# Kernel tuning notes

Measured on AMD Instinct MI355X. Metric: run time of the kernel, lower is better.

## Reference

```python
import jax, jax.numpy as jnp
import numpy as np

N = 100000   # total nodes across the batch of glycan graphs
E = 300000   # directed edges
H = 256      # hidden_dim
D = 128      # embedding_dim (projection out)
L = 3        # num_layers
G = 10000    # number of graphs in the batch
V = 14       # monosaccharide vocab size
EPS = 1e-5   # BatchNorm eps


def setup_inputs() -> dict:
    key = jax.random.key(0)
    ks = jax.random.split(key, 12)
    s = 1.0 / np.sqrt(H)
    node_ids = jax.random.randint(ks[0], (N,), 0, V, dtype=jnp.int32)
    edge_index = jax.random.randint(ks[1], (2, E), 0, N, dtype=jnp.int32)
    batch_ids = jnp.sort(jax.random.randint(ks[2], (N,), 0, G, dtype=jnp.int32))
    return {
        "node_ids": node_ids,
        "edge_index": edge_index,
        "batch_ids": batch_ids,
        "emb": jax.random.normal(ks[3], (V, H), jnp.float32),
        "Ws": jax.random.normal(ks[4], (L, H, H), jnp.float32) * s,
        "bs": jax.random.normal(ks[5], (L, H), jnp.float32) * 0.01,
        "gammas": 1.0 + 0.1 * jax.random.normal(ks[6], (L, H), jnp.float32),
        "betas": 0.1 * jax.random.normal(ks[7], (L, H), jnp.float32),
        "run_mean": 0.1 * jax.random.normal(ks[8], (L, H), jnp.float32),
        "run_var": jax.random.uniform(ks[9], (L, H), jnp.float32) + 0.5,
        "projW": jax.random.normal(ks[10], (H, D), jnp.float32) * s,
        "projb": jax.random.normal(ks[11], (D,), jnp.float32) * 0.01,
    }


def reference(node_ids, edge_index, batch_ids, emb, Ws, bs, gammas, betas,
              run_mean, run_var, projW, projb):
    # --- GCN normalization with self-loops (PyG GCNConv defaults) ---
    src, dst = edge_index[0], edge_index[1]
    loops = jnp.arange(N, dtype=src.dtype)
    src_f = jnp.concatenate([src, loops])  # [E+N]
    dst_f = jnp.concatenate([dst, loops])
    deg = jax.ops.segment_sum(jnp.ones_like(dst_f, dtype=jnp.float32), dst_f,
                              num_segments=N)
    dinv = jnp.where(deg > 0, jax.lax.rsqrt(deg), 0.0)
    norm = dinv[src_f] * dinv[dst_f]       # [E+N]

    x = emb[node_ids]                       # [N, H]
    for l in range(L):
        h = x @ Ws[l]                       # GCNConv linear transform
        msg = h[src_f] * norm[:, None]      # [E+N, H] gathered messages
        h = jax.ops.segment_sum(msg, dst_f, num_segments=N) + bs[l]
        # BatchNorm1d (eval mode: running stats) + ReLU; dropout is identity in eval
        h = (h - run_mean[l]) * jax.lax.rsqrt(run_var[l] + EPS) * gammas[l] + betas[l]
        x = jax.nn.relu(h)

    # global_mean_pool over graph assignment
    counts = jax.ops.segment_sum(jnp.ones((N,), jnp.float32), batch_ids,
                                 num_segments=G)
    sums = jax.ops.segment_sum(x, batch_ids, num_segments=G)   # [G, H]
    pooled = sums / jnp.maximum(counts, 1.0)[:, None]
    return pooled @ projW + projb           # [G, D]
```

## Files before the change

kernel.cpp:

```cpp
#include <hip/hip_runtime.h>

#define HDIM 256
#define DDIM 128
#define VSZ 14

typedef __bf16 bf16x8 __attribute__((ext_vector_type(8)));
typedef float f32x4 __attribute__((ext_vector_type(4)));

static __device__ __forceinline__ unsigned short f2bf(float f) {
  unsigned u = __builtin_bit_cast(unsigned, f);
  u += 0x7FFF + ((u >> 16) & 1);
  return (unsigned short)(u >> 16);
}
static __device__ __forceinline__ unsigned pack2(float a, float b) {
  return (unsigned)f2bf(a) | ((unsigned)f2bf(b) << 16);
}
static __device__ __forceinline__ void ub8(uint4 p, float* o) {
  o[0] = __builtin_bit_cast(float, p.x << 16);
  o[1] = __builtin_bit_cast(float, p.x & 0xFFFF0000u);
  o[2] = __builtin_bit_cast(float, p.y << 16);
  o[3] = __builtin_bit_cast(float, p.y & 0xFFFF0000u);
  o[4] = __builtin_bit_cast(float, p.z << 16);
  o[5] = __builtin_bit_cast(float, p.z & 0xFFFF0000u);
  o[6] = __builtin_bit_cast(float, p.w << 16);
  o[7] = __builtin_bit_cast(float, p.w & 0xFFFF0000u);
}


__global__ void k_count(const int* __restrict__ dst, int* __restrict__ cnt, int E) {
  int i = blockIdx.x * 256 + threadIdx.x;
  if (i < E) atomicAdd(&cnt[dst[i]], 1);
}

__global__ void k_alloc(const int* __restrict__ cnt, int* __restrict__ off,
                        float* __restrict__ dinv, int2* __restrict__ ninfo,
                        const int* __restrict__ ids, int* __restrict__ total, int n) {
  __shared__ int s[256];
  __shared__ int base;
  int i = blockIdx.x * 256 + threadIdx.x;
  int c = (i < n) ? cnt[i] : 0;
  if (i < n) {
    float dv = rsqrtf((float)(c + 1));
    dinv[i] = dv;
    int2 inf;
    inf.x = ids[i];
    inf.y = __builtin_bit_cast(int, dv);
    ninfo[i] = inf;
  }
  s[threadIdx.x] = c;
  __syncthreads();
  for (int d = 1; d < 256; d <<= 1) {
    int add = (threadIdx.x >= d) ? s[threadIdx.x - d] : 0;
    __syncthreads();
    s[threadIdx.x] += add;
    __syncthreads();
  }
  if (threadIdx.x == 255) base = atomicAdd(total, s[255]);
  __syncthreads();
  if (i < n) off[i] = base + s[threadIdx.x] - c;
}

__global__ void k_fill(const int* __restrict__ src, const int* __restrict__ dst,
                       const int2* __restrict__ ninfo, const int* __restrict__ off,
                       int* __restrict__ cur, int4* __restrict__ edata, int E) {
  int i = blockIdx.x * 256 + threadIdx.x;
  if (i >= E) return;
  int d = dst[i];
  int p = off[d] + atomicAdd(&cur[d], 1);
  int s = src[i];
  int2 inf = ninfo[s];
  int4 v;
  v.x = s;
  v.y = inf.x;
  v.z = inf.y;
  v.w = 0;
  edata[p] = v;
}


__global__ __launch_bounds__(256) void k_prep(
    const float* __restrict__ emb, const float* __restrict__ Ws,
    const float* __restrict__ bs, const float* __restrict__ gam,
    const float* __restrict__ bet, const float* __restrict__ mu,
    const float* __restrict__ va, const int* __restrict__ batch,
    float* __restrict__ embW, float* __restrict__ Ac, float* __restrict__ Bc,
    unsigned short* __restrict__ Wtb, int* __restrict__ goff, int G, int n) {
  int b = blockIdx.x;
  if (b < 128) {
    __shared__ float tile[32][33];
    int layer = b >> 6;
    int tb = b & 63;
    int bx = (tb & 7) * 32, by = (tb >> 3) * 32;
    const float* W = Ws + (size_t)(layer + 1) * HDIM * HDIM;
    unsigned short* Wt = Wtb + (size_t)layer * HDIM * HDIM;
    int tx = threadIdx.x & 31, ty = threadIdx.x >> 5;
#pragma unroll
    for (int i = 0; i < 4; ++i)
      tile[ty + i * 8][tx] = W[(size_t)(by + ty + i * 8) * HDIM + bx + tx];
    __syncthreads();
#pragma unroll
    for (int i = 0; i < 4; ++i)
      Wt[(size_t)(bx + ty + i * 8) * HDIM + by + tx] = f2bf(tile[tx][ty + i * 8]);
  } else if (b < 142) {
    int t = b - 128, j = threadIdx.x;
    float acc = 0.f;
    for (int k = 0; k < HDIM; ++k) acc = fmaf(emb[t * HDIM + k], Ws[k * HDIM + j], acc);
    embW[t * HDIM + j] = acc;
  } else if (b < 145) {
    int i = (b - 142) * HDIM + threadIdx.x;
    float a = gam[i] * rsqrtf(va[i] + 1e-5f);
    Ac[i] = a;
    Bc[i] = (bs[i] - mu[i]) * a + bet[i];
  } else {
    int g = (b - 145) * 256 + threadIdx.x;
    if (g > G) return;
    int lo = 0, hi = n;
    while (lo < hi) {
      int mid = (lo + hi) >> 1;
      if (batch[mid] < g) lo = mid + 1;
      else hi = mid;
    }
    goff[g] = lo;
  }
}


__global__ __launch_bounds__(256) void k_layer1(
    const int* __restrict__ ids, const float* __restrict__ embW,
    const int* __restrict__ off, const int* __restrict__ deg,
    const int4* __restrict__ edata, const float* __restrict__ dinv,
    const float* __restrict__ A, const float* __restrict__ B,
    unsigned short* __restrict__ Y, int n) {
  __shared__ unsigned short lw[VSZ * HDIM];
  for (int i = threadIdx.x; i < VSZ * HDIM; i += 256) lw[i] = f2bf(embW[i]);
  __syncthreads();
  int j = (threadIdx.x & 31) * 8;
  float4 a0 = *reinterpret_cast<const float4*>(&A[j]);
  float4 a1 = *reinterpret_cast<const float4*>(&A[j + 4]);
  float4 b0 = *reinterpret_cast<const float4*>(&B[j]);
  float4 b1 = *reinterpret_cast<const float4*>(&B[j + 4]);
  int nb = (n + 7) >> 3;
  for (int b = blockIdx.x; b < nb; b += gridDim.x) {
    int v = b * 8 + (threadIdx.x >> 5);
    if (v >= n) continue;
    float dv = dinv[v];
    float s = dv * dv;
    float acc[8], m[8];
    uint4 x = *reinterpret_cast<const uint4*>(&lw[ids[v] * HDIM + j]);
    ub8(x, acc);
#pragma unroll
    for (int i = 0; i < 8; ++i) acc[i] *= s;
    int e = off[v], e1 = e + deg[v];
    for (; e + 3 < e1; e += 4) {
      int4 d0 = edata[e], d1 = edata[e + 1], d2 = edata[e + 2], d3 = edata[e + 3];
      uint4 g0 = *reinterpret_cast<const uint4*>(&lw[d0.y * HDIM + j]);
      uint4 g1 = *reinterpret_cast<const uint4*>(&lw[d1.y * HDIM + j]);
      uint4 g2 = *reinterpret_cast<const uint4*>(&lw[d2.y * HDIM + j]);
      uint4 g3 = *reinterpret_cast<const uint4*>(&lw[d3.y * HDIM + j]);
      float w0 = dv * __builtin_bit_cast(float, d0.z);
      float w1 = dv * __builtin_bit_cast(float, d1.z);
      float w2 = dv * __builtin_bit_cast(float, d2.z);
      float w3 = dv * __builtin_bit_cast(float, d3.z);
      ub8(g0, m);
#pragma unroll
      for (int i = 0; i < 8; ++i) acc[i] = fmaf(w0, m[i], acc[i]);
      ub8(g1, m);
#pragma unroll
      for (int i = 0; i < 8; ++i) acc[i] = fmaf(w1, m[i], acc[i]);
      ub8(g2, m);
#pragma unroll
      for (int i = 0; i < 8; ++i) acc[i] = fmaf(w2, m[i], acc[i]);
      ub8(g3, m);
#pragma unroll
      for (int i = 0; i < 8; ++i) acc[i] = fmaf(w3, m[i], acc[i]);
    }
    for (; e < e1; ++e) {
      int4 d0 = edata[e];
      uint4 g0 = *reinterpret_cast<const uint4*>(&lw[d0.y * HDIM + j]);
      float w0 = dv * __builtin_bit_cast(float, d0.z);
      ub8(g0, m);
#pragma unroll
      for (int i = 0; i < 8; ++i) acc[i] = fmaf(w0, m[i], acc[i]);
    }
    float o[8];
    o[0] = fmaxf(fmaf(acc[0], a0.x, b0.x), 0.f);
    o[1] = fmaxf(fmaf(acc[1], a0.y, b0.y), 0.f);
    o[2] = fmaxf(fmaf(acc[2], a0.z, b0.z), 0.f);
    o[3] = fmaxf(fmaf(acc[3], a0.w, b0.w), 0.f);
    o[4] = fmaxf(fmaf(acc[4], a1.x, b1.x), 0.f);
    o[5] = fmaxf(fmaf(acc[5], a1.y, b1.y), 0.f);
    o[6] = fmaxf(fmaf(acc[6], a1.z, b1.z), 0.f);
    o[7] = fmaxf(fmaf(acc[7], a1.w, b1.w), 0.f);
    uint4 st;
    st.x = pack2(o[0], o[1]);
    st.y = pack2(o[2], o[3]);
    st.z = pack2(o[4], o[5]);
    st.w = pack2(o[6], o[7]);
    *reinterpret_cast<uint4*>(&Y[(size_t)v * HDIM + j]) = st;
  }
}


__global__ __launch_bounds__(256) void k_agg(
    const unsigned short* __restrict__ X, const int* __restrict__ off,
    const int* __restrict__ deg, const int4* __restrict__ edata,
    const float* __restrict__ dinv, unsigned short* __restrict__ Yb, int n) {
  int j = (threadIdx.x & 31) * 8;
  int nb = (n + 7) >> 3;
  for (int b = blockIdx.x; b < nb; b += gridDim.x) {
    int v = b * 8 + (threadIdx.x >> 5);
    if (v >= n) continue;
    float dv = dinv[v];
    float s = dv * dv;
    float acc[8], m[8];
    uint4 x = *reinterpret_cast<const uint4*>(&X[(size_t)v * HDIM + j]);
    ub8(x, acc);
#pragma unroll
    for (int i = 0; i < 8; ++i) acc[i] *= s;
    int e = off[v], e1 = e + deg[v];
    for (; e + 3 < e1; e += 4) {
      int4 d0 = edata[e], d1 = edata[e + 1], d2 = edata[e + 2], d3 = edata[e + 3];
      uint4 g0 = *reinterpret_cast<const uint4*>(&X[(size_t)d0.x * HDIM + j]);
      uint4 g1 = *reinterpret_cast<const uint4*>(&X[(size_t)d1.x * HDIM + j]);
      uint4 g2 = *reinterpret_cast<const uint4*>(&X[(size_t)d2.x * HDIM + j]);
      uint4 g3 = *reinterpret_cast<const uint4*>(&X[(size_t)d3.x * HDIM + j]);
      float w0 = dv * __builtin_bit_cast(float, d0.z);
      float w1 = dv * __builtin_bit_cast(float, d1.z);
      float w2 = dv * __builtin_bit_cast(float, d2.z);
      float w3 = dv * __builtin_bit_cast(float, d3.z);
      ub8(g0, m);
#pragma unroll
      for (int i = 0; i < 8; ++i) acc[i] = fmaf(w0, m[i], acc[i]);
      ub8(g1, m);
#pragma unroll
      for (int i = 0; i < 8; ++i) acc[i] = fmaf(w1, m[i], acc[i]);
      ub8(g2, m);
#pragma unroll
      for (int i = 0; i < 8; ++i) acc[i] = fmaf(w2, m[i], acc[i]);
      ub8(g3, m);
#pragma unroll
      for (int i = 0; i < 8; ++i) acc[i] = fmaf(w3, m[i], acc[i]);
    }
    for (; e < e1; ++e) {
      int4 d0 = edata[e];
      uint4 g0 = *reinterpret_cast<const uint4*>(&X[(size_t)d0.x * HDIM + j]);
      float w0 = dv * __builtin_bit_cast(float, d0.z);
      ub8(g0, m);
#pragma unroll
      for (int i = 0; i < 8; ++i) acc[i] = fmaf(w0, m[i], acc[i]);
    }
    uint4 st;
    st.x = pack2(acc[0], acc[1]);
    st.y = pack2(acc[2], acc[3]);
    st.z = pack2(acc[4], acc[5]);
    st.w = pack2(acc[6], acc[7]);
    *reinterpret_cast<uint4*>(&Yb[(size_t)v * HDIM + j]) = st;
  }
}


#define BM 128
#define BN 128
#define BK 32
#define LDK 40
#define LDC 136

__global__ __launch_bounds__(256) void k_gemm_mfma(
    const unsigned short* __restrict__ Xb, const unsigned short* __restrict__ Wt,
    const float* __restrict__ Asc, const float* __restrict__ Bsh,
    unsigned short* __restrict__ Y, int M) {
  __shared__ uint4 smem4[BM * LDC / 8];
  unsigned short* As = reinterpret_cast<unsigned short*>(smem4);
  unsigned short* Bs = As + BM * LDK;
  unsigned short* Cs = As;
  int t = threadIdx.x;
  int m0 = blockIdx.x * BM;
  int n0 = blockIdx.y * BN;
  int l = t & 63, w = t >> 6;
  int wm = w & 1, wn = w >> 1;
  int cl = l & 15, q = l >> 4;
  int r0 = t >> 2;
  int kc = (t & 3) * 8;

  f32x4 acc[4][4];
  f32x4 zf = {0.f, 0.f, 0.f, 0.f};
#pragma unroll
  for (int i = 0; i < 4; ++i)
#pragma unroll
    for (int jj = 0; jj < 4; ++jj) acc[i][jj] = zf;

  int arow0 = m0 + r0;      if (arow0 > M - 1) arow0 = M - 1;
  int arow1 = m0 + r0 + 64; if (arow1 > M - 1) arow1 = M - 1;
  int brow0 = n0 + r0, brow1 = n0 + r0 + 64;

  for (int k0 = 0; k0 < HDIM; k0 += BK) {
    uint4 a0 = *reinterpret_cast<const uint4*>(&Xb[(size_t)arow0 * HDIM + k0 + kc]);
    uint4 a1 = *reinterpret_cast<const uint4*>(&Xb[(size_t)arow1 * HDIM + k0 + kc]);
    uint4 b0 = *reinterpret_cast<const uint4*>(&Wt[(size_t)brow0 * HDIM + k0 + kc]);
    uint4 b1 = *reinterpret_cast<const uint4*>(&Wt[(size_t)brow1 * HDIM + k0 + kc]);
    __syncthreads();
    *reinterpret_cast<uint4*>(&As[r0 * LDK + kc]) = a0;
    *reinterpret_cast<uint4*>(&As[(r0 + 64) * LDK + kc]) = a1;
    *reinterpret_cast<uint4*>(&Bs[r0 * LDK + kc]) = b0;
    *reinterpret_cast<uint4*>(&Bs[(r0 + 64) * LDK + kc]) = b1;
    __syncthreads();
    bf16x8 af[4], bfr[4];
#pragma unroll
    for (int i = 0; i < 4; ++i)
      af[i] = *reinterpret_cast<const bf16x8*>(&As[(wm * 64 + i * 16 + cl) * LDK + q * 8]);
#pragma unroll
    for (int jj = 0; jj < 4; ++jj)
      bfr[jj] = *reinterpret_cast<const bf16x8*>(&Bs[(wn * 64 + jj * 16 + cl) * LDK + q * 8]);
#pragma unroll
    for (int i = 0; i < 4; ++i)
#pragma unroll
      for (int jj = 0; jj < 4; ++jj)
        acc[i][jj] = __builtin_amdgcn_mfma_f32_16x16x32_bf16(af[i], bfr[jj], acc[i][jj], 0, 0, 0);
  }

  __syncthreads();
#pragma unroll
  for (int jj = 0; jj < 4; ++jj) {
    int col = wn * 64 + jj * 16 + cl;
    float as = Asc[n0 + col], bsv = Bsh[n0 + col];
#pragma unroll
    for (int i = 0; i < 4; ++i) {
      int rowb = wm * 64 + i * 16 + q * 4;
#pragma unroll
      for (int r = 0; r < 4; ++r)
        Cs[(rowb + r) * LDC + col] = f2bf(fmaxf(fmaf(acc[i][jj][r], as, bsv), 0.f));
    }
  }
  __syncthreads();
#pragma unroll
  for (int c = 0; c < 8; ++c) {
    int idx = t + 256 * c;
    int row = idx >> 4, cq = (idx & 15) * 8;
    int gr = m0 + row;
    if (gr < M)
      *reinterpret_cast<uint4*>(&Y[(size_t)gr * HDIM + n0 + cq]) =
          *reinterpret_cast<const uint4*>(&Cs[row * LDC + cq]);
  }
}


__global__ __launch_bounds__(256) void k_pool(
    const unsigned short* __restrict__ X, const int* __restrict__ goff,
    float* __restrict__ P, int G) {
  int g = blockIdx.x * 8 + (threadIdx.x >> 5);
  if (g >= G) return;
  int j = (threadIdx.x & 31) * 8;
  int r0 = goff[g], r1 = goff[g + 1];
  float acc[8] = {0.f, 0.f, 0.f, 0.f, 0.f, 0.f, 0.f, 0.f};
  float m[8];
  int r = r0;
  for (; r + 1 < r1; r += 2) {
    uint4 x0 = *reinterpret_cast<const uint4*>(&X[(size_t)r * HDIM + j]);
    uint4 x1 = *reinterpret_cast<const uint4*>(&X[(size_t)(r + 1) * HDIM + j]);
    ub8(x0, m);
#pragma unroll
    for (int i = 0; i < 8; ++i) acc[i] += m[i];
    ub8(x1, m);
#pragma unroll
    for (int i = 0; i < 8; ++i) acc[i] += m[i];
  }
  if (r < r1) {
    uint4 x0 = *reinterpret_cast<const uint4*>(&X[(size_t)r * HDIM + j]);
    ub8(x0, m);
#pragma unroll
    for (int i = 0; i < 8; ++i) acc[i] += m[i];
  }
  float inv = 1.f / fmaxf((float)(r1 - r0), 1.f);
  float4 o0 = make_float4(acc[0] * inv, acc[1] * inv, acc[2] * inv, acc[3] * inv);
  float4 o1 = make_float4(acc[4] * inv, acc[5] * inv, acc[6] * inv, acc[7] * inv);
  *reinterpret_cast<float4*>(&P[(size_t)g * HDIM + j]) = o0;
  *reinterpret_cast<float4*>(&P[(size_t)g * HDIM + j + 4]) = o1;
}


__global__ __launch_bounds__(128) void k_proj(
    const float* __restrict__ P, const float* __restrict__ W,
    const float* __restrict__ bias, float* __restrict__ out, int G) {
  __shared__ float rows[8][HDIM];
  int g0 = blockIdx.x * 8;
  for (int i = threadIdx.x; i < 8 * HDIM; i += 128) {
    int g = g0 + (i >> 8);
    rows[i >> 8][i & 255] = (g < G) ? P[(size_t)g * HDIM + (i & 255)] : 0.f;
  }
  __syncthreads();
  int d = threadIdx.x;
  float bb = bias[d];
  float acc[8] = {bb, bb, bb, bb, bb, bb, bb, bb};
  for (int k = 0; k < HDIM; ++k) {
    float w = W[(size_t)k * DDIM + d];
#pragma unroll
    for (int q = 0; q < 8; ++q) acc[q] = fmaf(rows[q][k], w, acc[q]);
  }
#pragma unroll
  for (int q = 0; q < 8; ++q) {
    int g = g0 + q;
    if (g < G) out[(size_t)g * DDIM + d] = acc[q];
  }
}


extern "C" void kernel_launch(void* const* d_in, const int* in_sizes, int n_in,
                              void* d_out, int out_size, void* d_ws, size_t ws_size,
                              hipStream_t stream) {
  const int N = in_sizes[0];
  const int E = in_sizes[1] / 2;
  const int G = out_size / DDIM;

  const int* node_ids = (const int*)d_in[0];
  const int* src = (const int*)d_in[1];
  const int* dst = src + E;
  const int* batch = (const int*)d_in[2];
  const float* emb = (const float*)d_in[3];
  const float* Ws = (const float*)d_in[4];
  const float* bs = (const float*)d_in[5];
  const float* gam = (const float*)d_in[6];
  const float* bet = (const float*)d_in[7];
  const float* mu = (const float*)d_in[8];
  const float* va = (const float*)d_in[9];
  const float* pW = (const float*)d_in[10];
  const float* pb = (const float*)d_in[11];
  float* out = (float*)d_out;

  size_t o = 0;
  auto alloc = [&](size_t bytes) -> void* {
    size_t start = (o + 255) & ~(size_t)255;
    o = start + bytes;
    return (void*)((char*)d_ws + start);
  };
  int* zbuf = (int*)alloc((size_t)(2 * N + 1) * 4);
  int* cnt = zbuf;
  int* cur = zbuf + N;
  int* total = zbuf + 2 * N;
  float* dinv = (float*)alloc((size_t)N * 4);
  int* off = (int*)alloc((size_t)N * 4);
  int2* ninfo = (int2*)alloc((size_t)N * 8);
  int4* edata = (int4*)alloc((size_t)E * 16);
  float* embW = (float*)alloc((size_t)VSZ * HDIM * 4);
  float* Ac = (float*)alloc((size_t)3 * HDIM * 4);
  float* Bc = (float*)alloc((size_t)3 * HDIM * 4);
  int* goff = (int*)alloc((size_t)(G + 1) * 4);
  unsigned short* Wtb = (unsigned short*)alloc((size_t)2 * HDIM * HDIM * 2);
  unsigned short* bufX = (unsigned short*)alloc((size_t)N * HDIM * 2);
  unsigned short* bufY = (unsigned short*)alloc((size_t)N * HDIM * 2);
  float* pooled = (float*)alloc((size_t)G * HDIM * 4);

  int gE = (E + 255) / 256;
  int NB = (N + 255) / 256;
  int NGB = (G + 1 + 255) / 256;

  hipMemsetAsync(zbuf, 0, (size_t)(2 * N + 1) * 4, stream);
  k_count<<<gE, 256, 0, stream>>>(dst, cnt, E);
  k_alloc<<<NB, 256, 0, stream>>>(cnt, off, dinv, ninfo, node_ids, total, N);
  k_fill<<<gE, 256, 0, stream>>>(src, dst, ninfo, off, cur, edata, E);

  k_prep<<<145 + NGB, 256, 0, stream>>>(emb, Ws, bs, gam, bet, mu, va, batch,
                                        embW, Ac, Bc, Wtb, goff, G, N);

  int gs = 2048;
  k_layer1<<<gs, 256, 0, stream>>>(node_ids, embW, off, cnt, edata, dinv,
                                   Ac, Bc, bufX, N);

  dim3 gg((N + BM - 1) / BM, HDIM / BN);
  k_agg<<<gs, 256, 0, stream>>>(bufX, off, cnt, edata, dinv, bufY, N);
  k_gemm_mfma<<<gg, 256, 0, stream>>>(bufY, Wtb, Ac + HDIM, Bc + HDIM, bufX, N);
  k_agg<<<gs, 256, 0, stream>>>(bufX, off, cnt, edata, dinv, bufY, N);
  k_gemm_mfma<<<gg, 256, 0, stream>>>(bufY, Wtb + HDIM * HDIM, Ac + 2 * HDIM, Bc + 2 * HDIM, bufX, N);

  k_pool<<<(G + 7) / 8, 256, 0, stream>>>(bufX, goff, pooled, G);
  k_proj<<<(G + 7) / 8, 128, 0, stream>>>(pooled, pW, pb, out, G);
}
```

Before: 270.7 us.

## Pack edge records to 8 bytes and fuse mean-pool into final GEMM epilogue

Edge records shrink from 16 to 8 bytes by packing the node id (24 bits) and the vocab id (top 8 bits) into one int, which halves edge-list traffic in the aggregation kernels. The last GEMM now skips writing its bf16 output and instead sums rows per graph from shared memory, adding the partial sums into a zeroed fp32 pooled buffer with atomics. The pool kernel is removed and the mean division moves into the projection kernel. This trades one full write and read of the node feature matrix for atomic contention and a larger memset, and it relies on node ids fitting in 24 bits.

```diff
diff --git a/kernel.cpp b/kernel.cpp
--- a/kernel.cpp
+++ b/kernel.cpp
@@ -11,6 +11,10 @@
   unsigned u = __builtin_bit_cast(unsigned, f);
   u += 0x7FFF + ((u >> 16) & 1);
   return (unsigned short)(u >> 16);
+}
+static __device__ __forceinline__ float bf2f(unsigned short u) {
+  unsigned x = ((unsigned)u) << 16;
+  return __builtin_bit_cast(float, x);
 }
 static __device__ __forceinline__ unsigned pack2(float a, float b) {
   return (unsigned)f2bf(a) | ((unsigned)f2bf(b) << 16);
@@ -62,18 +66,16 @@
 
 __global__ void k_fill(const int* __restrict__ src, const int* __restrict__ dst,
                        const int2* __restrict__ ninfo, const int* __restrict__ off,
-                       int* __restrict__ cur, int4* __restrict__ edata, int E) {
+                       int* __restrict__ cur, int2* __restrict__ edata, int E) {
   int i = blockIdx.x * 256 + threadIdx.x;
   if (i >= E) return;
   int d = dst[i];
   int p = off[d] + atomicAdd(&cur[d], 1);
   int s = src[i];
   int2 inf = ninfo[s];
-  int4 v;
-  v.x = s;
-  v.y = inf.x;
-  v.z = inf.y;
-  v.w = 0;
+  int2 v;
+  v.x = s | (inf.x << 24);
+  v.y = inf.y;
   edata[p] = v;
 }
 
@@ -128,7 +130,7 @@
 __global__ __launch_bounds__(256) void k_layer1(
     const int* __restrict__ ids, const float* __restrict__ embW,
     const int* __restrict__ off, const int* __restrict__ deg,
-    const int4* __restrict__ edata, const float* __restrict__ dinv,
+    const int2* __restrict__ edata, const float* __restrict__ dinv,
     const float* __restrict__ A, const float* __restrict__ B,
     unsigned short* __restrict__ Y, int n) {
   __shared__ unsigned short lw[VSZ * HDIM];
@@ -152,15 +154,15 @@
     for (int i = 0; i < 8; ++i) acc[i] *= s;
     int e = off[v], e1 = e + deg[v];
     for (; e + 3 < e1; e += 4) {
-      int4 d0 = edata[e], d1 = edata[e + 1], d2 = edata[e + 2], d3 = edata[e + 3];
-      uint4 g0 = *reinterpret_cast<const uint4*>(&lw[d0.y * HDIM + j]);
-      uint4 g1 = *reinterpret_cast<const uint4*>(&lw[d1.y * HDIM + j]);
-      uint4 g2 = *reinterpret_cast<const uint4*>(&lw[d2.y * HDIM + j]);
-      uint4 g3 = *reinterpret_cast<const uint4*>(&lw[d3.y * HDIM + j]);
-      float w0 = dv * __builtin_bit_cast(float, d0.z);
-      float w1 = dv * __builtin_bit_cast(float, d1.z);
-      float w2 = dv * __builtin_bit_cast(float, d2.z);
-      float w3 = dv * __builtin_bit_cast(float, d3.z);
+      int2 d0 = edata[e], d1 = edata[e + 1], d2 = edata[e + 2], d3 = edata[e + 3];
+      uint4 g0 = *reinterpret_cast<const uint4*>(&lw[((unsigned)d0.x >> 24) * HDIM + j]);
+      uint4 g1 = *reinterpret_cast<const uint4*>(&lw[((unsigned)d1.x >> 24) * HDIM + j]);
+      uint4 g2 = *reinterpret_cast<const uint4*>(&lw[((unsigned)d2.x >> 24) * HDIM + j]);
+      uint4 g3 = *reinterpret_cast<const uint4*>(&lw[((unsigned)d3.x >> 24) * HDIM + j]);
+      float w0 = dv * __builtin_bit_cast(float, d0.y);
+      float w1 = dv * __builtin_bit_cast(float, d1.y);
+      float w2 = dv * __builtin_bit_cast(float, d2.y);
+      float w3 = dv * __builtin_bit_cast(float, d3.y);
       ub8(g0, m);
 #pragma unroll
       for (int i = 0; i < 8; ++i) acc[i] = fmaf(w0, m[i], acc[i]);
@@ -175,9 +177,9 @@
       for (int i = 0; i < 8; ++i) acc[i] = fmaf(w3, m[i], acc[i]);
     }
     for (; e < e1; ++e) {
-      int4 d0 = edata[e];
-      uint4 g0 = *reinterpret_cast<const uint4*>(&lw[d0.y * HDIM + j]);
-      float w0 = dv * __builtin_bit_cast(float, d0.z);
+      int2 d0 = edata[e];
+      uint4 g0 = *reinterpret_cast<const uint4*>(&lw[((unsigned)d0.x >> 24) * HDIM + j]);
+      float w0 = dv * __builtin_bit_cast(float, d0.y);
       ub8(g0, m);
 #pragma unroll
       for (int i = 0; i < 8; ++i) acc[i] = fmaf(w0, m[i], acc[i]);
@@ -203,7 +205,7 @@
 
 __global__ __launch_bounds__(256) void k_agg(
     const unsigned short* __restrict__ X, const int* __restrict__ off,
-    const int* __restrict__ deg, const int4* __restrict__ edata,
+    const int* __restrict__ deg, const int2* __restrict__ edata,
     const float* __restrict__ dinv, unsigned short* __restrict__ Yb, int n) {
   int j = (threadIdx.x & 31) * 8;
   int nb = (n + 7) >> 3;
@@ -219,15 +221,15 @@
     for (int i = 0; i < 8; ++i) acc[i] *= s;
     int e = off[v], e1 = e + deg[v];
     for (; e + 3 < e1; e += 4) {
-      int4 d0 = edata[e], d1 = edata[e + 1], d2 = edata[e + 2], d3 = edata[e + 3];
-      uint4 g0 = *reinterpret_cast<const uint4*>(&X[(size_t)d0.x * HDIM + j]);
-      uint4 g1 = *reinterpret_cast<const uint4*>(&X[(size_t)d1.x * HDIM + j]);
-      uint4 g2 = *reinterpret_cast<const uint4*>(&X[(size_t)d2.x * HDIM + j]);
-      uint4 g3 = *reinterpret_cast<const uint4*>(&X[(size_t)d3.x * HDIM + j]);
-      float w0 = dv * __builtin_bit_cast(float, d0.z);
-      float w1 = dv * __builtin_bit_cast(float, d1.z);
-      float w2 = dv * __builtin_bit_cast(float, d2.z);
-      float w3 = dv * __builtin_bit_cast(float, d3.z);
+      int2 d0 = edata[e], d1 = edata[e + 1], d2 = edata[e + 2], d3 = edata[e + 3];
+      uint4 g0 = *reinterpret_cast<const uint4*>(&X[(size_t)(d0.x & 0xFFFFFF) * HDIM + j]);
+      uint4 g1 = *reinterpret_cast<const uint4*>(&X[(size_t)(d1.x & 0xFFFFFF) * HDIM + j]);
+      uint4 g2 = *reinterpret_cast<const uint4*>(&X[(size_t)(d2.x & 0xFFFFFF) * HDIM + j]);
+      uint4 g3 = *reinterpret_cast<const uint4*>(&X[(size_t)(d3.x & 0xFFFFFF) * HDIM + j]);
+      float w0 = dv * __builtin_bit_cast(float, d0.y);
+      float w1 = dv * __builtin_bit_cast(float, d1.y);
+      float w2 = dv * __builtin_bit_cast(float, d2.y);
+      float w3 = dv * __builtin_bit_cast(float, d3.y);
       ub8(g0, m);
 #pragma unroll
       for (int i = 0; i < 8; ++i) acc[i] = fmaf(w0, m[i], acc[i]);
@@ -242,9 +244,9 @@
       for (int i = 0; i < 8; ++i) acc[i] = fmaf(w3, m[i], acc[i]);
     }
     for (; e < e1; ++e) {
-      int4 d0 = edata[e];
-      uint4 g0 = *reinterpret_cast<const uint4*>(&X[(size_t)d0.x * HDIM + j]);
-      float w0 = dv * __builtin_bit_cast(float, d0.z);
+      int2 d0 = edata[e];
+      uint4 g0 = *reinterpret_cast<const uint4*>(&X[(size_t)(d0.x & 0xFFFFFF) * HDIM + j]);
+      float w0 = dv * __builtin_bit_cast(float, d0.y);
       ub8(g0, m);
 #pragma unroll
       for (int i = 0; i < 8; ++i) acc[i] = fmaf(w0, m[i], acc[i]);
@@ -265,10 +267,12 @@
 #define LDK 40
 #define LDC 136
 
+template <bool POOL>
 __global__ __launch_bounds__(256) void k_gemm_mfma(
     const unsigned short* __restrict__ Xb, const unsigned short* __restrict__ Wt,
     const float* __restrict__ Asc, const float* __restrict__ Bsh,
-    unsigned short* __restrict__ Y, int M) {
+    unsigned short* __restrict__ Y, float* __restrict__ pooled,
+    const int* __restrict__ batch, int M) {
   __shared__ uint4 smem4[BM * LDC / 8];
   unsigned short* As = reinterpret_cast<unsigned short*>(smem4);
   unsigned short* Bs = As + BM * LDK;
@@ -332,60 +336,54 @@
     }
   }
   __syncthreads();
-#pragma unroll
-  for (int c = 0; c < 8; ++c) {
-    int idx = t + 256 * c;
-    int row = idx >> 4, cq = (idx & 15) * 8;
-    int gr = m0 + row;
-    if (gr < M)
-      *reinterpret_cast<uint4*>(&Y[(size_t)gr * HDIM + n0 + cq]) =
-          *reinterpret_cast<const uint4*>(&Cs[row * LDC + cq]);
-  }
-}
-
-
-__global__ __launch_bounds__(256) void k_pool(
-    const unsigned short* __restrict__ X, const int* __restrict__ goff,
-    float* __restrict__ P, int G) {
-  int g = blockIdx.x * 8 + (threadIdx.x >> 5);
-  if (g >= G) return;
-  int j = (threadIdx.x & 31) * 8;
-  int r0 = goff[g], r1 = goff[g + 1];
-  float acc[8] = {0.f, 0.f, 0.f, 0.f, 0.f, 0.f, 0.f, 0.f};
-  float m[8];
-  int r = r0;
-  for (; r + 1 < r1; r += 2) {
-    uint4 x0 = *reinterpret_cast<const uint4*>(&X[(size_t)r * HDIM + j]);
-    uint4 x1 = *reinterpret_cast<const uint4*>(&X[(size_t)(r + 1) * HDIM + j]);
-    ub8(x0, m);
-#pragma unroll
-    for (int i = 0; i < 8; ++i) acc[i] += m[i];
-    ub8(x1, m);
-#pragma unroll
-    for (int i = 0; i < 8; ++i) acc[i] += m[i];
-  }
-  if (r < r1) {
-    uint4 x0 = *reinterpret_cast<const uint4*>(&X[(size_t)r * HDIM + j]);
-    ub8(x0, m);
-#pragma unroll
-    for (int i = 0; i < 8; ++i) acc[i] += m[i];
-  }
-  float inv = 1.f / fmaxf((float)(r1 - r0), 1.f);
-  float4 o0 = make_float4(acc[0] * inv, acc[1] * inv, acc[2] * inv, acc[3] * inv);
-  float4 o1 = make_float4(acc[4] * inv, acc[5] * inv, acc[6] * inv, acc[7] * inv);
-  *reinterpret_cast<float4*>(&P[(size_t)g * HDIM + j]) = o0;
-  *reinterpret_cast<float4*>(&P[(size_t)g * HDIM + j + 4]) = o1;
+  if (!POOL) {
+#pragma unroll
+    for (int c = 0; c < 8; ++c) {
+      int idx = t + 256 * c;
+      int row = idx >> 4, cq = (idx & 15) * 8;
+      int gr = m0 + row;
+      if (gr < M)
+        *reinterpret_cast<uint4*>(&Y[(size_t)gr * HDIM + n0 + cq]) =
+            *reinterpret_cast<const uint4*>(&Cs[row * LDC + cq]);
+    }
+  } else {
+    int col = t & 127;
+    int rbeg = (t >> 7) * 64;
+    float sum = 0.f;
+    int gprev = -1;
+    for (int r = rbeg; r < rbeg + 64; ++r) {
+      int gr = m0 + r;
+      if (gr >= M) break;
+      int g = batch[gr];
+      if (g != gprev) {
+        if (gprev >= 0) atomicAdd(&pooled[(size_t)gprev * HDIM + n0 + col], sum);
+        sum = 0.f;
+        gprev = g;
+      }
+      sum += bf2f(Cs[r * LDC + col]);
+    }
+    if (gprev >= 0) atomicAdd(&pooled[(size_t)gprev * HDIM + n0 + col], sum);
+  }
 }
 
 
 __global__ __launch_bounds__(128) void k_proj(
-    const float* __restrict__ P, const float* __restrict__ W,
-    const float* __restrict__ bias, float* __restrict__ out, int G) {
+    const float* __restrict__ P, const int* __restrict__ goff,
+    const float* __restrict__ W, const float* __restrict__ bias,
+    float* __restrict__ out, int G) {
   __shared__ float rows[8][HDIM];
+  __shared__ float sinv[8];
   int g0 = blockIdx.x * 8;
+  if (threadIdx.x < 8) {
+    int g = g0 + threadIdx.x;
+    float c = (g < G) ? (float)(goff[g + 1] - goff[g]) : 1.f;
+    sinv[threadIdx.x] = 1.f / fmaxf(c, 1.f);
+  }
+  __syncthreads();
   for (int i = threadIdx.x; i < 8 * HDIM; i += 128) {
-    int g = g0 + (i >> 8);
-    rows[i >> 8][i & 255] = (g < G) ? P[(size_t)g * HDIM + (i & 255)] : 0.f;
+    int qg = i >> 8;
+    int g = g0 + qg;
+    rows[qg][i & 255] = (g < G) ? P[(size_t)g * HDIM + (i & 255)] * sinv[qg] : 0.f;
   }
   __syncthreads();
   int d = threadIdx.x;
@@ -436,10 +434,12 @@
   int* cnt = zbuf;
   int* cur = zbuf + N;
   int* total = zbuf + 2 * N;
+  float* pooled = (float*)alloc((size_t)G * HDIM * 4);
+  size_t zbytes = (size_t)((char*)pooled - (char*)zbuf) + (size_t)G * HDIM * 4;
   float* dinv = (float*)alloc((size_t)N * 4);
   int* off = (int*)alloc((size_t)N * 4);
   int2* ninfo = (int2*)alloc((size_t)N * 8);
-  int4* edata = (int4*)alloc((size_t)E * 16);
+  int2* edata = (int2*)alloc((size_t)E * 8);
   float* embW = (float*)alloc((size_t)VSZ * HDIM * 4);
   float* Ac = (float*)alloc((size_t)3 * HDIM * 4);
   float* Bc = (float*)alloc((size_t)3 * HDIM * 4);
@@ -447,13 +447,12 @@
   unsigned short* Wtb = (unsigned short*)alloc((size_t)2 * HDIM * HDIM * 2);
   unsigned short* bufX = (unsigned short*)alloc((size_t)N * HDIM * 2);
   unsigned short* bufY = (unsigned short*)alloc((size_t)N * HDIM * 2);
-  float* pooled = (float*)alloc((size_t)G * HDIM * 4);
 
   int gE = (E + 255) / 256;
   int NB = (N + 255) / 256;
   int NGB = (G + 1 + 255) / 256;
 
-  hipMemsetAsync(zbuf, 0, (size_t)(2 * N + 1) * 4, stream);
+  hipMemsetAsync(zbuf, 0, zbytes, stream);
   k_count<<<gE, 256, 0, stream>>>(dst, cnt, E);
   k_alloc<<<NB, 256, 0, stream>>>(cnt, off, dinv, ninfo, node_ids, total, N);
   k_fill<<<gE, 256, 0, stream>>>(src, dst, ninfo, off, cur, edata, E);
@@ -467,10 +466,11 @@
 
   dim3 gg((N + BM - 1) / BM, HDIM / BN);
   k_agg<<<gs, 256, 0, stream>>>(bufX, off, cnt, edata, dinv, bufY, N);
-  k_gemm_mfma<<<gg, 256, 0, stream>>>(bufY, Wtb, Ac + HDIM, Bc + HDIM, bufX, N);
+  k_gemm_mfma<false><<<gg, 256, 0, stream>>>(bufY, Wtb, Ac + HDIM, Bc + HDIM,
+                                             bufX, pooled, batch, N);
   k_agg<<<gs, 256, 0, stream>>>(bufX, off, cnt, edata, dinv, bufY, N);
-  k_gemm_mfma<<<gg, 256, 0, stream>>>(bufY, Wtb + HDIM * HDIM, Ac + 2 * HDIM, Bc + 2 * HDIM, bufX, N);
-
-  k_pool<<<(G + 7) / 8, 256, 0, stream>>>(bufX, goff, pooled, G);
-  k_proj<<<(G + 7) / 8, 128, 0, stream>>>(pooled, pW, pb, out, G);
-}
+  k_gemm_mfma<true><<<gg, 256, 0, stream>>>(bufY, Wtb + HDIM * HDIM, Ac + 2 * HDIM,
+                                            Bc + 2 * HDIM, bufX, pooled, batch, N);
+
+  k_proj<<<(G + 7) / 8, 128, 0, stream>>>(pooled, goff, pW, pb, out, G);
+}
```

After: 296.1 us. 9.4% more time.
